# Kernel tuning notes

Hardware: AMD Instinct MI355X
Metric: run time of the kernel (lower is better)

The kernel has to match this reference:

```python
import jax, jax.numpy as jnp
import numpy as np

B, S, H = 1, 4096, 2048
NH, NKV = 16, 4
HD = H // NH  # 128
GROUPS = NH // NKV


def setup_inputs() -> dict:
    key = jax.random.key(0)
    ks = jax.random.split(key, 5)
    hidden_states = jax.random.normal(ks[0], (B, S, H), dtype=jnp.float32)
    # causal additive mask: 0 on/below diagonal, large negative above
    neg = jnp.finfo(jnp.float32).min
    causal = jnp.where(jnp.tril(jnp.ones((S, S), dtype=bool)), 0.0, neg)
    attention_mask = jnp.broadcast_to(causal, (B, 1, S, S)).astype(jnp.float32)
    sc = 0.02
    Wq = jax.random.normal(ks[1], (H, NH * HD), dtype=jnp.float32) * sc
    Wk = jax.random.normal(ks[2], (H, NKV * HD), dtype=jnp.float32) * sc
    Wv = jax.random.normal(ks[3], (H, NKV * HD), dtype=jnp.float32) * sc
    Wo = jax.random.normal(ks[4], (H, H), dtype=jnp.float32) * sc
    return {"hidden_states": hidden_states, "attention_mask": attention_mask,
            "Wq": Wq, "Wk": Wk, "Wv": Wv, "Wo": Wo}


def reference(hidden_states, attention_mask, Wq, Wk, Wv, Wo):
    b, s, _ = hidden_states.shape
    # projections -> (b, heads, s, hd)
    q = (hidden_states @ Wq).reshape(b, s, NH, HD).transpose(0, 2, 1, 3)
    k = (hidden_states @ Wk).reshape(b, s, NKV, HD).transpose(0, 2, 1, 3)
    v = (hidden_states @ Wv).reshape(b, s, NKV, HD).transpose(0, 2, 1, 3)
    # repeat_kv for GQA: (b, nkv, s, hd) -> (b, nh, s, hd)
    k = jnp.repeat(k, GROUPS, axis=1)
    v = jnp.repeat(v, GROUPS, axis=1)
    scores = jnp.einsum('bhqd,bhkd->bhqk', q, k) / jnp.sqrt(jnp.float32(HD))
    scores = scores + attention_mask
    attn = jax.nn.softmax(scores.astype(jnp.float32), axis=-1).astype(q.dtype)
    out = jnp.einsum('bhqk,bhkd->bhqd', attn, v)
    out = out.transpose(0, 2, 1, 3).reshape(b, s, H)
    return out @ Wo
```

## Files before the change

### kernel.cpp

```cpp
#include <hip/hip_runtime.h>


typedef __bf16 bf16;
typedef float f32x4 __attribute__((ext_vector_type(4)));
typedef float f32x16 __attribute__((ext_vector_type(16)));
typedef bf16 bf16x4 __attribute__((ext_vector_type(4)));
typedef bf16 bf16x8 __attribute__((ext_vector_type(8)));
typedef unsigned u32x4 __attribute__((ext_vector_type(4)));

#define MFMA16(A, B, C) __builtin_amdgcn_mfma_f32_16x16x32_bf16((A), (B), (C), 0, 0, 0)
#define MFMA32(A, B, C) __builtin_amdgcn_mfma_f32_32x32x16_bf16((A), (B), (C), 0, 0, 0)

__device__ __forceinline__ void async16(const bf16* g, bf16* l) {
  __builtin_amdgcn_global_load_lds(
      (const __attribute__((address_space(1))) unsigned int*)g,
      (__attribute__((address_space(3))) unsigned int*)l, 16, 0, 0);
}

__device__ __forceinline__ float exp2v(float x) {
  float r; asm("v_exp_f32 %0, %1" : "=v"(r) : "v"(x)); return r;
}
__device__ __forceinline__ unsigned cvtpk(float a, float b) {
  unsigned r; asm("v_cvt_pk_bf16_f32 %0, %1, %2" : "=v"(r) : "v"(a), "v"(b)); return r;
}
#define PLSWAP(a, b) asm("v_permlane32_swap_b32 %0, %1" : "+v"(a), "+v"(b))

__device__ __forceinline__ bf16x8 mkfrag(unsigned a0, unsigned a1,
                                         unsigned c0, unsigned c1) {
  PLSWAP(a0, c0);
  PLSWAP(a1, c1);
  u32x4 t = {a0, a1, c0, c1};
  return __builtin_bit_cast(bf16x8, t);
}

__global__ void cast_bf16_kernel(const float* __restrict__ in,
                                 bf16* __restrict__ out, int n4) {
  int i = blockIdx.x * blockDim.x + threadIdx.x;
  int stride = gridDim.x * blockDim.x;
  for (; i < n4; i += stride) {
    float4 v = ((const float4*)in)[i];
    bf16x4 o = {(bf16)v.x, (bf16)v.y, (bf16)v.z, (bf16)v.w};
    ((bf16x4*)out)[i] = o;
  }
}

__global__ void transpose_cast_kernel(const float* __restrict__ src, int srcCols,
                                      bf16* __restrict__ dst, float scale) {
  __shared__ float t[64][65];
  const int kt = blockIdx.y * 64;
  const int nt = blockIdx.x * 64;
  const int r0 = threadIdx.x >> 4;
  const int c0 = (threadIdx.x & 15) * 4;
#pragma unroll
  for (int i = 0; i < 4; ++i) {
    int r = r0 + i * 16;
    float4 v = *(const float4*)(src + (kt + r) * srcCols + nt + c0);
    t[r][c0 + 0] = v.x; t[r][c0 + 1] = v.y; t[r][c0 + 2] = v.z; t[r][c0 + 3] = v.w;
  }
  __syncthreads();
#pragma unroll
  for (int i = 0; i < 4; ++i) {
    int r = r0 + i * 16;
    bf16x4 b = {(bf16)(t[c0 + 0][r] * scale), (bf16)(t[c0 + 1][r] * scale),
                (bf16)(t[c0 + 2][r] * scale), (bf16)(t[c0 + 3][r] * scale)};
    *(bf16x4*)(dst + (nt + r) * 2048 + kt + c0) = b;
  }
}

template <int MODE>
__global__ __launch_bounds__(256, 2) void gemm_bt(
    const bf16* __restrict__ A, const bf16* __restrict__ BT, int K,
    bf16* __restrict__ Qb, bf16* __restrict__ Kb, bf16* __restrict__ Vt,
    float* __restrict__ Cf) {
  __shared__ bf16 As[128 * 32];
  __shared__ bf16 Bs[128 * 32];
  const int tid = threadIdx.x;
  const int w = tid >> 6, lane = tid & 63, g = lane >> 4, lq = lane & 15;
  const int wr = w >> 1, wc = w & 1;
  const int mBase = blockIdx.y * 128, nBase = blockIdx.x * 128;

  f32x4 acc[4][4] = {};
  const int KT = K >> 5;
  for (int kt = 0; kt < KT; ++kt) {
#pragma unroll
    for (int r = 0; r < 2; ++r) {
      int chunk = r * 256 + tid;
      int row = chunk >> 2, cu = chunk & 3;
      async16(A + (mBase + row) * K + kt * 32 + cu * 8, As + (r * 256 + w * 64) * 8);
      async16(BT + (nBase + row) * K + kt * 32 + cu * 8, Bs + (r * 256 + w * 64) * 8);
    }
    asm volatile("s_waitcnt vmcnt(0)" ::: "memory");
    __syncthreads();

    bf16x8 af[4], bfr[4];
#pragma unroll
    for (int i = 0; i < 4; ++i)
      af[i] = *(const bf16x8*)(As + (wr * 64 + i * 16 + lq) * 32 + g * 8);
#pragma unroll
    for (int i = 0; i < 4; ++i)
      bfr[i] = *(const bf16x8*)(Bs + (wc * 64 + i * 16 + lq) * 32 + g * 8);
#pragma unroll
    for (int mi = 0; mi < 4; ++mi)
#pragma unroll
      for (int ni = 0; ni < 4; ++ni)
        acc[mi][ni] = MFMA16(af[mi], bfr[ni], acc[mi][ni]);
    __syncthreads();
  }

#pragma unroll
  for (int mi = 0; mi < 4; ++mi)
#pragma unroll
    for (int ni = 0; ni < 4; ++ni) {
      const int n = nBase + wc * 64 + ni * 16 + lq;
      const int m0 = mBase + wr * 64 + mi * 16 + 4 * g;
      if (MODE == 0) {
        if (nBase < 2048) {
#pragma unroll
          for (int jr = 0; jr < 4; ++jr)
            Qb[(m0 + jr) * 2048 + n] = (bf16)acc[mi][ni][jr];
        } else if (nBase < 2560) {
#pragma unroll
          for (int jr = 0; jr < 4; ++jr)
            Kb[(m0 + jr) * 512 + (n - 2048)] = (bf16)acc[mi][ni][jr];
        } else {
          bf16x4 v = {(bf16)acc[mi][ni][0], (bf16)acc[mi][ni][1],
                      (bf16)acc[mi][ni][2], (bf16)acc[mi][ni][3]};
          *(bf16x4*)(Vt + (n - 2560) * 4096 + m0) = v;
        }
      } else {
#pragma unroll
        for (int jr = 0; jr < 4; ++jr)
          Cf[(m0 + jr) * 2048 + n] = acc[mi][ni][jr];
      }
    }
}

__global__ __launch_bounds__(256, 2) void attn_fwd(
    const bf16* __restrict__ Qb,
    const bf16* __restrict__ Kb,
    const bf16* __restrict__ Vt,
    bf16* __restrict__ AO) {
  __shared__ __align__(16) bf16 Ks[2][64 * 128];
  __shared__ __align__(16) bf16 Vs[2][128 * 64];

  const int bid = blockIdx.x;
  const int h = bid & 15;
  const int qt = (bid < 256) ? (bid >> 4) : (31 - ((bid - 256) >> 4));
  const int kv = h >> 2;
  const int tid = threadIdx.x;
  const int w = tid >> 6, lane = tid & 63, l5 = lane & 31, g2 = lane >> 5;
  const int sxr = (l5 & 7) << 4;
  const int qbase = qt * 128;
  const int nk = 2 * (qt + 1);
  const int qw = qbase + w * 32 + l5;

  bf16x8 aq[8];
  {
    const bf16* qrow = Qb + qw * 2048 + h * 128;
#pragma unroll
    for (int kk = 0; kk < 8; ++kk)
      aq[kk] = *(const bf16x8*)(qrow + kk * 16 + g2 * 8);
  }

  float mst = -1e30f, lst = 0.f;
  f32x16 o[4] = {};

  auto STAGE_K = [&](int t, int buf) {
#pragma unroll
    for (int r = 0; r < 4; ++r) {
      int gid = r * 256 + tid;
      int krow = gid >> 4, cu = gid & 15;
      async16(Kb + (t * 64 + krow) * 512 + kv * 128 + ((cu ^ (krow & 7)) * 8),
              &Ks[buf][(r * 256 + w * 64) * 8]);
    }
  };
  auto STAGE_V = [&](int t, int buf) {
#pragma unroll
    for (int r = 0; r < 4; ++r) {
      int gid = r * 256 + tid;
      int vrow = gid >> 3, gv = gid & 7;
      async16(Vt + (kv * 128 + vrow) * 4096 + t * 64 + ((gv ^ (vrow & 7)) * 8),
              &Vs[buf][(r * 256 + w * 64) * 8]);
    }
  };

  STAGE_K(0, 0);
  STAGE_V(0, 0);
  STAGE_K(1, 1);
  asm volatile("s_waitcnt vmcnt(8)" ::: "memory");
  __builtin_amdgcn_s_barrier();
  __builtin_amdgcn_sched_barrier(0);

  f32x16 s0 = {}, s1 = {};
  {
    const char* kb0 = (const char*)&Ks[0][0] + l5 * 256;
    __builtin_amdgcn_s_setprio(1);
#pragma unroll
    for (int kk = 0; kk < 8; ++kk) {
      const int off = (kk * 32 + g2 * 16) ^ sxr;
      bf16x8 k0 = *(const bf16x8*)(kb0 + off);
      bf16x8 k1 = *(const bf16x8*)(kb0 + 8192 + off);
      s0 = MFMA32(k0, aq[kk], s0);
      s1 = MFMA32(k1, aq[kk], s1);
    }
    __builtin_amdgcn_s_setprio(0);
  }
  __builtin_amdgcn_sched_barrier(0);
  __builtin_amdgcn_s_barrier();

  for (int t = 0; t < nk; ++t) {
    const int cur = t & 1, nxt = (t + 1) & 1;

    if (t >= 2 * qt) {
      const int kb = t * 64 + 4 * g2;
#pragma unroll
      for (int r = 0; r < 16; ++r) {
        const int key = kb + (r & 3) + 8 * (r >> 2);
        if (key > qw) s0[r] = -1e30f;
        if (key + 32 > qw) s1[r] = -1e30f;
      }
    }

    {
      float mx[16];
#pragma unroll
      for (int r = 0; r < 16; ++r) mx[r] = fmaxf(s0[r], s1[r]);
#pragma unroll
      for (int off = 8; off > 0; off >>= 1)
#pragma unroll
        for (int r = 0; r < off; ++r) mx[r] = fmaxf(mx[r], mx[r + off]);
      const float pm = fmaxf(mx[0], __shfl_xor(mx[0], 32));

      if (__any(pm > mst + 8.f)) {
        const float mn = fmaxf(mst, pm);
        const float al = exp2v(mst - mn);
        mst = mn;
        lst *= al;
#pragma unroll
        for (int dt = 0; dt < 4; ++dt)
#pragma unroll
          for (int r = 0; r < 16; ++r) o[dt][r] *= al;
      }
#pragma unroll
      for (int r = 0; r < 16; ++r) {
        s0[r] = exp2v(s0[r] - mst);
        s1[r] = exp2v(s1[r] - mst);
      }
      float sm[16];
#pragma unroll
      for (int r = 0; r < 16; ++r) sm[r] = s0[r] + s1[r];
#pragma unroll
      for (int off = 8; off > 0; off >>= 1)
#pragma unroll
        for (int r = 0; r < off; ++r) sm[r] += sm[r + off];
      lst += sm[0] + __shfl_xor(sm[0], 32);
    }

    bf16x8 pb[4];
    {
      unsigned pw0[8], pw1[8];
#pragma unroll
      for (int wi = 0; wi < 8; ++wi) {
        pw0[wi] = cvtpk(s0[2 * wi], s0[2 * wi + 1]);
        pw1[wi] = cvtpk(s1[2 * wi], s1[2 * wi + 1]);
      }
      pb[0] = mkfrag(pw0[0], pw0[1], pw0[2], pw0[3]);
      pb[1] = mkfrag(pw0[4], pw0[5], pw0[6], pw0[7]);
      pb[2] = mkfrag(pw1[0], pw1[1], pw1[2], pw1[3]);
      pb[3] = mkfrag(pw1[4], pw1[5], pw1[6], pw1[7]);
    }

    STAGE_K(min(t + 2, nk - 1), cur);
    STAGE_V(min(t + 1, nk - 1), nxt);
    asm volatile("s_waitcnt vmcnt(8)" ::: "memory");
    __builtin_amdgcn_s_barrier();
    __builtin_amdgcn_sched_barrier(0);

    f32x16 n0 = {}, n1 = {};
    const char* kb0 = (const char*)&Ks[nxt][0] + l5 * 256;
    const char* vb0 = (const char*)&Vs[cur][0];
    if (t + 1 < nk) {
      __builtin_amdgcn_s_setprio(1);
#pragma unroll
      for (int i = 0; i < 8; ++i) {
        const int koff = (i * 32 + g2 * 16) ^ sxr;
        bf16x8 k0 = *(const bf16x8*)(kb0 + koff);
        bf16x8 k1 = *(const bf16x8*)(kb0 + 8192 + koff);
        n0 = MFMA32(k0, aq[i], n0);
        n1 = MFMA32(k1, aq[i], n1);
        {
          const int j = 2 * i, dt = j & 3, KK = j >> 2;
          bf16x8 av = *(const bf16x8*)(vb0 + (dt * 32 + l5) * 128 +
                                       ((KK * 32 + g2 * 16) ^ sxr));
          o[dt] = MFMA32(av, pb[KK], o[dt]);
        }
        {
          const int j = 2 * i + 1, dt = j & 3, KK = j >> 2;
          bf16x8 av = *(const bf16x8*)(vb0 + (dt * 32 + l5) * 128 +
                                       ((KK * 32 + g2 * 16) ^ sxr));
          o[dt] = MFMA32(av, pb[KK], o[dt]);
        }
      }
      __builtin_amdgcn_s_setprio(0);
    } else {
      __builtin_amdgcn_s_setprio(1);
#pragma unroll
      for (int j = 0; j < 16; ++j) {
        const int dt = j & 3, KK = j >> 2;
        bf16x8 av = *(const bf16x8*)(vb0 + (dt * 32 + l5) * 128 +
                                     ((KK * 32 + g2 * 16) ^ sxr));
        o[dt] = MFMA32(av, pb[KK], o[dt]);
      }
      __builtin_amdgcn_s_setprio(0);
    }
    __builtin_amdgcn_sched_barrier(0);
    __builtin_amdgcn_s_barrier();

    s0 = n0;
    s1 = n1;
  }

  {
    const float inv = 1.f / lst;
    bf16* aob = AO + qw * 2048 + h * 128;
#pragma unroll
    for (int dt = 0; dt < 4; ++dt)
#pragma unroll
      for (int m = 0; m < 4; ++m) {
        bf16x4 ov = {(bf16)(o[dt][4 * m + 0] * inv), (bf16)(o[dt][4 * m + 1] * inv),
                     (bf16)(o[dt][4 * m + 2] * inv), (bf16)(o[dt][4 * m + 3] * inv)};
        *(bf16x4*)(aob + dt * 32 + 8 * m + 4 * g2) = ov;
      }
  }
}

extern "C" void kernel_launch(void* const* d_in, const int* in_sizes, int n_in,
                              void* d_out, int out_size, void* d_ws, size_t ws_size,
                              hipStream_t stream) {
  const float* X = (const float*)d_in[0];
  const float* Wq = (const float*)d_in[2];
  const float* Wk = (const float*)d_in[3];
  const float* Wv = (const float*)d_in[4];
  const float* Wo = (const float*)d_in[5];
  float* out = (float*)d_out;
  char* ws = (char*)d_ws;

  bf16* Xb = (bf16*)ws;
  bf16* WT = (bf16*)(ws + 16777216);
  bf16* Qb = (bf16*)(ws + 29360128);
  bf16* Kb = (bf16*)(ws + 46137344);
  bf16* Vt = (bf16*)(ws + 50331648);

  cast_bf16_kernel<<<2048, 256, 0, stream>>>(X, Xb, (4096 * 2048) / 4);
  transpose_cast_kernel<<<dim3(32, 32), 256, 0, stream>>>(
      Wq, 2048, WT, 0.08838834764831845f * 1.4426950408889634f);
  transpose_cast_kernel<<<dim3(8, 32), 256, 0, stream>>>(Wk, 512, WT + 2048 * 2048, 1.0f);
  transpose_cast_kernel<<<dim3(8, 32), 256, 0, stream>>>(Wv, 512, WT + 2560 * 2048, 1.0f);

  gemm_bt<0><<<dim3(24, 32), 256, 0, stream>>>(Xb, WT, 2048, Qb, Kb, Vt, (float*)nullptr);

  transpose_cast_kernel<<<dim3(32, 32), 256, 0, stream>>>(Wo, 2048, WT, 1.0f);

  attn_fwd<<<512, 256, 0, stream>>>(Qb, Kb, Vt, Xb);

  gemm_bt<1><<<dim3(16, 32), 256, 0, stream>>>(Xb, WT, 2048, (bf16*)nullptr,
                                               (bf16*)nullptr, (bf16*)nullptr, out);
}
```

Baseline: 258.0 us.

## Shrink attention tiles to 64 queries and 32-key blocks with 2-wave CTAs

The attention kernel moves from 128-query, 4-wave blocks with 64-key tiles to 64-query, 2-wave blocks with 32-key tiles, launching 1024 blocks instead of 512. Shared-memory buffers and the LDS swizzle for V are reworked to match, and the softmax and masking loops now handle a single score accumulator. The aim is finer causal granularity, less wasted masked work and more blocks per CU for better balance. In exchange, each K/V tile is reused by fewer query rows and there are more barrier and loop iterations per unit of work.

```diff
diff --git a/kernel.cpp b/kernel.cpp
--- a/kernel.cpp
+++ b/kernel.cpp
@@ -135,22 +135,21 @@
     }
 }
 
-__global__ __launch_bounds__(256, 2) void attn_fwd(
+__global__ __launch_bounds__(128, 4) void attn_fwd(
     const bf16* __restrict__ Qb,
     const bf16* __restrict__ Kb,
     const bf16* __restrict__ Vt,
     bf16* __restrict__ AO) {
-  __shared__ __align__(16) bf16 Ks[2][64 * 128];
-  __shared__ __align__(16) bf16 Vs[2][128 * 64];
+  __shared__ __align__(16) bf16 Ks[2][32 * 128];
+  __shared__ __align__(16) bf16 Vs[2][128 * 32];
 
   const int bid = blockIdx.x;
   const int h = bid & 15;
-  const int qt = (bid < 256) ? (bid >> 4) : (31 - ((bid - 256) >> 4));
+  const int qt = (bid < 512) ? (bid >> 4) : (63 - ((bid - 512) >> 4));
   const int kv = h >> 2;
   const int tid = threadIdx.x;
   const int w = tid >> 6, lane = tid & 63, l5 = lane & 31, g2 = lane >> 5;
-  const int sxr = (l5 & 7) << 4;
-  const int qbase = qt * 128;
+  const int qbase = qt * 64;
   const int nk = 2 * (qt + 1);
   const int qw = qbase + w * 32 + l5;
 
@@ -168,21 +167,24 @@
   auto STAGE_K = [&](int t, int buf) {
 #pragma unroll
     for (int r = 0; r < 4; ++r) {
-      int gid = r * 256 + tid;
+      int gid = r * 128 + tid;
       int krow = gid >> 4, cu = gid & 15;
-      async16(Kb + (t * 64 + krow) * 512 + kv * 128 + ((cu ^ (krow & 7)) * 8),
-              &Ks[buf][(r * 256 + w * 64) * 8]);
+      async16(Kb + (t * 32 + krow) * 512 + kv * 128 + ((cu ^ (krow & 7)) * 8),
+              &Ks[buf][(r * 128 + w * 64) * 8]);
     }
   };
   auto STAGE_V = [&](int t, int buf) {
 #pragma unroll
     for (int r = 0; r < 4; ++r) {
-      int gid = r * 256 + tid;
-      int vrow = gid >> 3, gv = gid & 7;
-      async16(Vt + (kv * 128 + vrow) * 4096 + t * 64 + ((gv ^ (vrow & 7)) * 8),
-              &Vs[buf][(r * 256 + w * 64) * 8]);
+      int gid = r * 128 + tid;
+      int vrow = gid >> 2, gv = gid & 3;
+      async16(Vt + (kv * 128 + vrow) * 4096 + t * 32 + ((gv ^ ((vrow >> 1) & 3)) * 8),
+              &Vs[buf][(r * 128 + w * 64) * 8]);
     }
   };
+
+  const int sxk = (l5 & 7);
+  const int sxv = ((l5 >> 1) & 3);
 
   STAGE_K(0, 0);
   STAGE_V(0, 0);
@@ -191,17 +193,14 @@
   __builtin_amdgcn_s_barrier();
   __builtin_amdgcn_sched_barrier(0);
 
-  f32x16 s0 = {}, s1 = {};
+  f32x16 s = {};
   {
     const char* kb0 = (const char*)&Ks[0][0] + l5 * 256;
     __builtin_amdgcn_s_setprio(1);
 #pragma unroll
     for (int kk = 0; kk < 8; ++kk) {
-      const int off = (kk * 32 + g2 * 16) ^ sxr;
-      bf16x8 k0 = *(const bf16x8*)(kb0 + off);
-      bf16x8 k1 = *(const bf16x8*)(kb0 + 8192 + off);
-      s0 = MFMA32(k0, aq[kk], s0);
-      s1 = MFMA32(k1, aq[kk], s1);
+      bf16x8 k0 = *(const bf16x8*)(kb0 + ((((kk << 1) | g2) ^ sxk) << 4));
+      s = MFMA32(k0, aq[kk], s);
     }
     __builtin_amdgcn_s_setprio(0);
   }
@@ -212,21 +211,20 @@
     const int cur = t & 1, nxt = (t + 1) & 1;
 
     if (t >= 2 * qt) {
-      const int kb = t * 64 + 4 * g2;
+      const int kb = t * 32 + 4 * g2;
 #pragma unroll
       for (int r = 0; r < 16; ++r) {
         const int key = kb + (r & 3) + 8 * (r >> 2);
-        if (key > qw) s0[r] = -1e30f;
-        if (key + 32 > qw) s1[r] = -1e30f;
+        if (key > qw) s[r] = -1e30f;
       }
     }
 
     {
-      float mx[16];
-#pragma unroll
-      for (int r = 0; r < 16; ++r) mx[r] = fmaxf(s0[r], s1[r]);
-#pragma unroll
-      for (int off = 8; off > 0; off >>= 1)
+      float mx[8];
+#pragma unroll
+      for (int r = 0; r < 8; ++r) mx[r] = fmaxf(s[r], s[r + 8]);
+#pragma unroll
+      for (int off = 4; off > 0; off >>= 1)
 #pragma unroll
         for (int r = 0; r < off; ++r) mx[r] = fmaxf(mx[r], mx[r + off]);
       const float pm = fmaxf(mx[0], __shfl_xor(mx[0], 32));
@@ -242,32 +240,24 @@
           for (int r = 0; r < 16; ++r) o[dt][r] *= al;
       }
 #pragma unroll
-      for (int r = 0; r < 16; ++r) {
-        s0[r] = exp2v(s0[r] - mst);
-        s1[r] = exp2v(s1[r] - mst);
-      }
-      float sm[16];
-#pragma unroll
-      for (int r = 0; r < 16; ++r) sm[r] = s0[r] + s1[r];
-#pragma unroll
-      for (int off = 8; off > 0; off >>= 1)
+      for (int r = 0; r < 16; ++r) s[r] = exp2v(s[r] - mst);
+      float sm[8];
+#pragma unroll
+      for (int r = 0; r < 8; ++r) sm[r] = s[r] + s[r + 8];
+#pragma unroll
+      for (int off = 4; off > 0; off >>= 1)
 #pragma unroll
         for (int r = 0; r < off; ++r) sm[r] += sm[r + off];
       lst += sm[0] + __shfl_xor(sm[0], 32);
     }
 
-    bf16x8 pb[4];
+    bf16x8 pb[2];
     {
-      unsigned pw0[8], pw1[8];
-#pragma unroll
-      for (int wi = 0; wi < 8; ++wi) {
-        pw0[wi] = cvtpk(s0[2 * wi], s0[2 * wi + 1]);
-        pw1[wi] = cvtpk(s1[2 * wi], s1[2 * wi + 1]);
-      }
-      pb[0] = mkfrag(pw0[0], pw0[1], pw0[2], pw0[3]);
-      pb[1] = mkfrag(pw0[4], pw0[5], pw0[6], pw0[7]);
-      pb[2] = mkfrag(pw1[0], pw1[1], pw1[2], pw1[3]);
-      pb[3] = mkfrag(pw1[4], pw1[5], pw1[6], pw1[7]);
+      unsigned pw[8];
+#pragma unroll
+      for (int wi = 0; wi < 8; ++wi) pw[wi] = cvtpk(s[2 * wi], s[2 * wi + 1]);
+      pb[0] = mkfrag(pw[0], pw[1], pw[2], pw[3]);
+      pb[1] = mkfrag(pw[4], pw[5], pw[6], pw[7]);
     }
 
     STAGE_K(min(t + 2, nk - 1), cur);
@@ -276,39 +266,28 @@
     __builtin_amdgcn_s_barrier();
     __builtin_amdgcn_sched_barrier(0);
 
-    f32x16 n0 = {}, n1 = {};
+    f32x16 n0 = {};
     const char* kb0 = (const char*)&Ks[nxt][0] + l5 * 256;
     const char* vb0 = (const char*)&Vs[cur][0];
     if (t + 1 < nk) {
       __builtin_amdgcn_s_setprio(1);
 #pragma unroll
       for (int i = 0; i < 8; ++i) {
-        const int koff = (i * 32 + g2 * 16) ^ sxr;
-        bf16x8 k0 = *(const bf16x8*)(kb0 + koff);
-        bf16x8 k1 = *(const bf16x8*)(kb0 + 8192 + koff);
+        bf16x8 k0 = *(const bf16x8*)(kb0 + ((((i << 1) | g2) ^ sxk) << 4));
         n0 = MFMA32(k0, aq[i], n0);
-        n1 = MFMA32(k1, aq[i], n1);
-        {
-          const int j = 2 * i, dt = j & 3, KK = j >> 2;
-          bf16x8 av = *(const bf16x8*)(vb0 + (dt * 32 + l5) * 128 +
-                                       ((KK * 32 + g2 * 16) ^ sxr));
-          o[dt] = MFMA32(av, pb[KK], o[dt]);
-        }
-        {
-          const int j = 2 * i + 1, dt = j & 3, KK = j >> 2;
-          bf16x8 av = *(const bf16x8*)(vb0 + (dt * 32 + l5) * 128 +
-                                       ((KK * 32 + g2 * 16) ^ sxr));
-          o[dt] = MFMA32(av, pb[KK], o[dt]);
-        }
+        const int dt = i & 3, KK = i >> 2;
+        bf16x8 av = *(const bf16x8*)(vb0 + (dt * 32 + l5) * 64 +
+                                     ((((KK << 1) | g2) ^ sxv) << 4));
+        o[dt] = MFMA32(av, pb[KK], o[dt]);
       }
       __builtin_amdgcn_s_setprio(0);
     } else {
       __builtin_amdgcn_s_setprio(1);
 #pragma unroll
-      for (int j = 0; j < 16; ++j) {
+      for (int j = 0; j < 8; ++j) {
         const int dt = j & 3, KK = j >> 2;
-        bf16x8 av = *(const bf16x8*)(vb0 + (dt * 32 + l5) * 128 +
-                                     ((KK * 32 + g2 * 16) ^ sxr));
+        bf16x8 av = *(const bf16x8*)(vb0 + (dt * 32 + l5) * 64 +
+                                     ((((KK << 1) | g2) ^ sxv) << 4));
         o[dt] = MFMA32(av, pb[KK], o[dt]);
       }
       __builtin_amdgcn_s_setprio(0);
@@ -316,8 +295,7 @@
     __builtin_amdgcn_sched_barrier(0);
     __builtin_amdgcn_s_barrier();
 
-    s0 = n0;
-    s1 = n1;
+    s = n0;
   }
 
   {
@@ -361,7 +339,7 @@
 
   transpose_cast_kernel<<<dim3(32, 32), 256, 0, stream>>>(Wo, 2048, WT, 1.0f);
 
-  attn_fwd<<<512, 256, 0, stream>>>(Qb, Kb, Vt, Xb);
+  attn_fwd<<<1024, 128, 0, stream>>>(Qb, Kb, Vt, Xb);
 
   gemm_bt<1><<<dim3(16, 32), 256, 0, stream>>>(Xb, WT, 2048, (bf16*)nullptr,
                                                (bf16*)nullptr, (bf16*)nullptr, out);
```

New measurement: 318.8 us. +23.5%, slower.
